# Kernel tuning notes

Measured on AMD Instinct MI355X. Metric: run time of the kernel, lower is better.

The kernel has to match this reference:

```python
import jax, jax.numpy as jnp
import numpy as np

B, T, C, H = 8, 2048, 1024, 64

def setup_inputs() -> dict:
    key = jax.random.key(0)
    kx, kq, kk, kv = jax.random.split(key, 4)
    scale = 1.0 / np.sqrt(C)
    return {
        "x": jax.random.normal(kx, (B, T, C), dtype=jnp.float32),
        "Wq": jax.random.normal(kq, (C, H), dtype=jnp.float32) * scale,
        "Wk": jax.random.normal(kk, (C, H), dtype=jnp.float32) * scale,
        "Wv": jax.random.normal(kv, (C, H), dtype=jnp.float32) * scale,
    }

def reference(x, Wq, Wk, Wv):
    # q,k,v: [B,T,H]
    q = jnp.einsum('btc,ch->bth', x, Wq)
    k = jnp.einsum('btc,ch->bth', x, Wk)
    v = jnp.einsum('btc,ch->bth', x, Wv)
    scale = k.shape[-1] ** -0.5
    wei = jnp.einsum('bth,bsh->bts', q, k) * scale  # [B,T,T]
    causal = jnp.tril(jnp.ones((x.shape[1], x.shape[1]), dtype=bool))
    wei = jnp.where(causal, wei, -jnp.inf)
    wei = jax.nn.softmax(wei, axis=-1)
    out = jnp.einsum('bts,bsh->bth', wei, v)  # [B,T,H]
    return out
```

## Files before the change

kernel.cpp:

```cpp
#include <hip/hip_runtime.h>

#define B_ 8
#define T_ 2048
#define C_ 1024
#define H_ 64

typedef __bf16 bf16x8 __attribute__((ext_vector_type(8)));
typedef float  f32x4  __attribute__((ext_vector_type(4)));
typedef unsigned short u16x8 __attribute__((ext_vector_type(8)));

__device__ __forceinline__ unsigned short f2bf(float f) {
    unsigned u = __builtin_bit_cast(unsigned, f);
    u += 0x8000u;
    return (unsigned short)(u >> 16);
}

__device__ __forceinline__ unsigned pack2(float lo, float hi) {
    unsigned a = __builtin_bit_cast(unsigned, lo) + 0x8000u;
    unsigned b = __builtin_bit_cast(unsigned, hi) + 0x8000u;
    return (a >> 16) | (b & 0xffff0000u);
}

union U8 { unsigned u32[4]; u16x8 v; };

__device__ __forceinline__ u16x8 cvt8(float4 f0, float4 f1) {
    U8 r;
    r.u32[0] = pack2(f0.x, f0.y);
    r.u32[1] = pack2(f0.z, f0.w);
    r.u32[2] = pack2(f1.x, f1.y);
    r.u32[3] = pack2(f1.z, f1.w);
    return r.v;
}

__device__ __forceinline__ bf16x8 load8_bf(const unsigned short* p) {
    return __builtin_bit_cast(bf16x8, *(const u16x8*)p);
}

__global__ void cast_weights(const float* __restrict__ Wq,
                             const float* __restrict__ Wk,
                             const float* __restrict__ Wv,
                             unsigned short* __restrict__ Wt) {
    int idx = blockIdx.x * blockDim.x + threadIdx.x;
    int w   = idx >> 16;
    int rem = idx & 0xffff;
    int c   = rem & (C_ - 1);
    int h   = rem >> 10;
    const float* W = (w == 0) ? Wq : (w == 1) ? Wk : Wv;
    Wt[(size_t)(w * H_ + h) * C_ + c] = f2bf(W[(size_t)c * H_ + h]);
}

#define ABUF (64 * 64)
#define BBUF (192 * 64)

__global__ __launch_bounds__(512) void qkv_proj(
        const float* __restrict__ x,
        const unsigned short* __restrict__ Wt,
        unsigned short* __restrict__ Qb,
        unsigned short* __restrict__ Kb,
        unsigned short* __restrict__ VTb) {
    __shared__ __attribute__((aligned(16))) unsigned short As_[2 * ABUF];
    __shared__ __attribute__((aligned(16))) unsigned short Bs_[2 * BBUF];

    const int tid  = threadIdx.x;
    const int wave = tid >> 6;
    const int lane = tid & 63;
    const int l16  = lane & 15;
    const int quad = lane >> 4;
    const int ms   = wave >> 1;
    const int nh   = wave & 1;
    const size_t r0 = (size_t)blockIdx.x * 64;

    const int sa_m = tid >> 3, sa_g = tid & 7;
    const float* sa_src = x + (r0 + sa_m) * C_ + sa_g * 8;
    const int sa_off = sa_m * 64 + ((sa_g ^ (sa_m & 7)) * 8);

    f32x4 acc[6];
#pragma unroll
    for (int i = 0; i < 6; i++) acc[i] = (f32x4){0.f, 0.f, 0.f, 0.f};

    const int sw = l16 & 7;

    {
        float4 f0 = *(const float4*)(sa_src);
        float4 f1 = *(const float4*)(sa_src + 4);
        *(u16x8*)(&As_[sa_off]) = cvt8(f0, f1);
#pragma unroll
        for (int p = 0; p < 3; p++) {
            u16x8 v = *(const u16x8*)(Wt + (size_t)(p * 64 + sa_m) * C_ + sa_g * 8);
            *(u16x8*)(&Bs_[p * 4096 + sa_off]) = v;
        }
    }
    __syncthreads();

    int cur = 0;
    for (int ks = 0; ks < 16; ks++) {
        const int k1 = (ks + 1) * 64;
        const bool more = (k1 < C_);
        float4 na0, na1;
        u16x8 nb0, nb1, nb2;
        if (more) {
            na0 = *(const float4*)(sa_src + k1);
            na1 = *(const float4*)(sa_src + k1 + 4);
            nb0 = *(const u16x8*)(Wt + (size_t)(0 * 64 + sa_m) * C_ + k1 + sa_g * 8);
            nb1 = *(const u16x8*)(Wt + (size_t)(1 * 64 + sa_m) * C_ + k1 + sa_g * 8);
            nb2 = *(const u16x8*)(Wt + (size_t)(2 * 64 + sa_m) * C_ + k1 + sa_g * 8);
        }
        const unsigned short* Ac = As_ + cur * ABUF;
        const unsigned short* Bc = Bs_ + cur * BBUF;
        const int arow = ms * 16 + l16;
        bf16x8 a0 = load8_bf(&Ac[arow * 64 + ((quad ^ sw) * 8)]);
        bf16x8 a1 = load8_bf(&Ac[arow * 64 + (((quad + 4) ^ sw) * 8)]);
#pragma unroll
        for (int i = 0; i < 6; i++) {
            int brow = (nh * 6 + i) * 16 + l16;
            bf16x8 b0 = load8_bf(&Bc[brow * 64 + ((quad ^ sw) * 8)]);
            bf16x8 b1 = load8_bf(&Bc[brow * 64 + (((quad + 4) ^ sw) * 8)]);
            acc[i] = __builtin_amdgcn_mfma_f32_16x16x32_bf16(a0, b0, acc[i], 0, 0, 0);
            acc[i] = __builtin_amdgcn_mfma_f32_16x16x32_bf16(a1, b1, acc[i], 0, 0, 0);
        }
        if (more) {
            const int nxt = cur ^ 1;
            *(u16x8*)(&As_[nxt * ABUF + sa_off]) = cvt8(na0, na1);
            *(u16x8*)(&Bs_[nxt * BBUF + 0 * 4096 + sa_off]) = nb0;
            *(u16x8*)(&Bs_[nxt * BBUF + 1 * 4096 + sa_off]) = nb1;
            *(u16x8*)(&Bs_[nxt * BBUF + 2 * 4096 + sa_off]) = nb2;
            __syncthreads();
            cur = nxt;
        }
    }

    const int mrow_base = (int)r0 + ms * 16 + quad * 4;
#pragma unroll
    for (int i = 0; i < 6; i++) {
        int nt = nh * 6 + i;
#pragma unroll
        for (int r = 0; r < 4; r++) {
            int row = mrow_base + r;
            unsigned short bv = f2bf(acc[i][r]);
            if (nt < 4) {
                Qb[(size_t)row * H_ + nt * 16 + l16] = bv;
            } else if (nt < 8) {
                Kb[(size_t)row * H_ + (nt - 4) * 16 + l16] = bv;
            } else {
                int h = (nt - 8) * 16 + l16;
                int b = row >> 11;
                int t = row & (T_ - 1);
                VTb[((size_t)b * H_ + h) * T_ + t] = bv;
            }
        }
    }
}

#define PROW 33
#define OMS  65

__global__ __launch_bounds__(512) void attn(
        const unsigned short* __restrict__ Qb,
        const unsigned short* __restrict__ Kb,
        const unsigned short* __restrict__ VTb,
        float* __restrict__ out) {
    __shared__ unsigned int ps_[8 * 16 * PROW];
    __shared__ float Om_[8 * 16 * OMS];
    __shared__ float mred_[8 * 16];
    __shared__ float lred_[8 * 16];

    const int tid  = threadIdx.x;
    const int wave = tid >> 6;
    const int lane = tid & 63;
    const int l16  = lane & 15;
    const int quad = lane >> 4;
    const int b    = blockIdx.x >> 7;
    const int qt   = blockIdx.x & 127;
    const int q0   = qt * 16;
    const int tdiag = qt >> 2;

    const unsigned short* qrow =
        Qb + ((size_t)b * T_ + q0 + l16) * H_ + quad * 8;
    bf16x8 qf0 = load8_bf(qrow);
    bf16x8 qf1 = load8_bf(qrow + 32);

    f32x4 o[4];
#pragma unroll
    for (int i = 0; i < 4; i++) o[i] = (f32x4){0.f, 0.f, 0.f, 0.f};
    float m_run = -1e30f, l_run = 0.f;

    const float scale = 0.125f;
    const unsigned short* Kbase = Kb + (size_t)b * T_ * H_;
    const unsigned short* Vbase = VTb + (size_t)b * H_ * T_;
    unsigned int* Pw = &ps_[wave * 16 * PROW];

    for (int t = wave; t <= tdiag; t += 8) {
        bf16x8 vf[8];
#pragma unroll
        for (int ht = 0; ht < 4; ht++)
#pragma unroll
            for (int ks = 0; ks < 2; ks++)
                vf[ht * 2 + ks] = load8_bf(
                    Vbase + (size_t)(ht * 16 + l16) * T_ + t * 64 + ks * 32 + quad * 8);

        f32x4 s[4];
#pragma unroll
        for (int nt = 0; nt < 4; nt++) {
            const unsigned short* krow =
                Kbase + (size_t)(t * 64 + nt * 16 + l16) * H_ + quad * 8;
            bf16x8 kf0 = load8_bf(krow);
            bf16x8 kf1 = load8_bf(krow + 32);
            f32x4 z = (f32x4){0.f, 0.f, 0.f, 0.f};
            z = __builtin_amdgcn_mfma_f32_16x16x32_bf16(kf0, qf0, z, 0, 0, 0);
            z = __builtin_amdgcn_mfma_f32_16x16x32_bf16(kf1, qf1, z, 0, 0, 0);
            s[nt] = z;
        }

#pragma unroll
        for (int nt = 0; nt < 4; nt++)
#pragma unroll
            for (int r = 0; r < 4; r++) s[nt][r] *= scale;

        if (t == tdiag) {
#pragma unroll
            for (int nt = 0; nt < 4; nt++) {
#pragma unroll
                for (int r = 0; r < 4; r++) {
                    int key = t * 64 + nt * 16 + quad * 4 + r;
                    if (key > q0 + l16) s[nt][r] = -1e30f;
                }
            }
        }

        float mx;
        {
            float m0 = fmaxf(fmaxf(s[0][0], s[0][1]), fmaxf(s[0][2], s[0][3]));
            float m1 = fmaxf(fmaxf(s[1][0], s[1][1]), fmaxf(s[1][2], s[1][3]));
            float m2 = fmaxf(fmaxf(s[2][0], s[2][1]), fmaxf(s[2][2], s[2][3]));
            float m3 = fmaxf(fmaxf(s[3][0], s[3][1]), fmaxf(s[3][2], s[3][3]));
            mx = fmaxf(fmaxf(m0, m1), fmaxf(m2, m3));
        }
        mx = fmaxf(mx, __shfl_xor(mx, 16));
        mx = fmaxf(mx, __shfl_xor(mx, 32));
        const float m_new = fmaxf(m_run, mx);
        const float alpha = __expf(m_run - m_new);
        m_run = m_new;

        float rs = 0.f;
#pragma unroll
        for (int nt = 0; nt < 4; nt++) {
#pragma unroll
            for (int i = 0; i < 2; i++) {
                float p0 = __expf(s[nt][2 * i]     - m_new);
                float p1 = __expf(s[nt][2 * i + 1] - m_new);
                rs += p0 + p1;
                Pw[l16 * PROW + nt * 8 + quad * 2 + i] = pack2(p0, p1);
            }
        }
        rs += __shfl_xor(rs, 16);
        rs += __shfl_xor(rs, 32);
        l_run = l_run * alpha + rs;

#pragma unroll
        for (int ht = 0; ht < 4; ht++)
#pragma unroll
            for (int r = 0; r < 4; r++) o[ht][r] *= alpha;

#pragma unroll
        for (int ks = 0; ks < 2; ks++) {
            bf16x8 pB = __builtin_bit_cast(bf16x8,
                *(const u16x8*)(&Pw[l16 * PROW + ks * 16 + quad * 4]));
#pragma unroll
            for (int ht = 0; ht < 4; ht++)
                o[ht] = __builtin_amdgcn_mfma_f32_16x16x32_bf16(
                    vf[ht * 2 + ks], pB, o[ht], 0, 0, 0);
        }
    }

#pragma unroll
    for (int ht = 0; ht < 4; ht++)
#pragma unroll
        for (int r = 0; r < 4; r++)
            Om_[(wave * 16 + l16) * OMS + ht * 16 + quad * 4 + r] = o[ht][r];
    if (quad == 0) {
        mred_[wave * 16 + l16] = m_run;
        lred_[wave * 16 + l16] = l_run;
    }
    __syncthreads();

    const int hcol = tid & 63;
    const int qrow0 = tid >> 6;
#pragma unroll
    for (int qq = 0; qq < 2; qq++) {
        const int q = qrow0 + qq * 8;
        float M = -1e30f;
#pragma unroll
        for (int w = 0; w < 8; w++) M = fmaxf(M, mred_[w * 16 + q]);
        float lt = 0.f, ov = 0.f;
#pragma unroll
        for (int w = 0; w < 8; w++) {
            float e = __expf(mred_[w * 16 + q] - M);
            lt += e * lred_[w * 16 + q];
            ov += e * Om_[(w * 16 + q) * OMS + hcol];
        }
        out[((size_t)b * T_ + q0 + q) * H_ + hcol] = ov / lt;
    }
}

extern "C" void kernel_launch(void* const* d_in, const int* in_sizes, int n_in,
                              void* d_out, int out_size, void* d_ws, size_t ws_size,
                              hipStream_t stream) {
    const float* x  = (const float*)d_in[0];
    const float* Wq = (const float*)d_in[1];
    const float* Wk = (const float*)d_in[2];
    const float* Wv = (const float*)d_in[3];
    float* out = (float*)d_out;

    unsigned short* Qb  = (unsigned short*)d_ws;
    unsigned short* Kb  = Qb  + (size_t)B_ * T_ * H_;
    unsigned short* VTb = Kb  + (size_t)B_ * T_ * H_;
    unsigned short* Wt  = VTb + (size_t)B_ * T_ * H_;

    cast_weights<<<(3 * C_ * H_) / 256, 256, 0, stream>>>(Wq, Wk, Wv, Wt);
    qkv_proj<<<(B_ * T_) / 64, 512, 0, stream>>>(x, Wt, Qb, Kb, VTb);
    attn<<<B_ * (T_ / 16), 512, 0, stream>>>(Qb, Kb, VTb, out);
}
```

Measured before the change: 163.7 us.

## Store Q/K/V in MFMA fragment-tiled layout and split projection across N halves

The projection kernel now writes Q, K and V directly in a tiled layout that matches the MFMA fragment order, so the attention kernel's loads become contiguous 1KB chunks instead of strided row reads. The projection grid is also restructured to 32-row, 96-column tiles with 256 threads, giving four times as many smaller blocks. Separately, the cross-wave output reduction buffer in shared memory is stored as bf16 instead of fp32 to cut LDS footprint. The trade-offs are the extra bf16 rounding in the final combine and the x rows being read twice by the two N-half blocks.

```diff
diff --git a/kernel.cpp b/kernel.cpp
--- a/kernel.cpp
+++ b/kernel.cpp
@@ -13,6 +13,11 @@
     unsigned u = __builtin_bit_cast(unsigned, f);
     u += 0x8000u;
     return (unsigned short)(u >> 16);
+}
+
+__device__ __forceinline__ float bf2f(unsigned short v) {
+    unsigned u = ((unsigned)v) << 16;
+    return __builtin_bit_cast(float, u);
 }
 
 __device__ __forceinline__ unsigned pack2(float lo, float hi) {
@@ -35,6 +40,7 @@
 __device__ __forceinline__ bf16x8 load8_bf(const unsigned short* p) {
     return __builtin_bit_cast(bf16x8, *(const u16x8*)p);
 }
+
 
 __global__ void cast_weights(const float* __restrict__ Wq,
                              const float* __restrict__ Wk,
@@ -49,15 +55,15 @@
     Wt[(size_t)(w * H_ + h) * C_ + c] = f2bf(W[(size_t)c * H_ + h]);
 }
 
-#define ABUF (64 * 64)
-#define BBUF (192 * 64)
-
-__global__ __launch_bounds__(512) void qkv_proj(
+#define ABUF 2048
+#define BBUF 6144
+
+__global__ __launch_bounds__(256) void qkv_proj(
         const float* __restrict__ x,
         const unsigned short* __restrict__ Wt,
-        unsigned short* __restrict__ Qb,
-        unsigned short* __restrict__ Kb,
-        unsigned short* __restrict__ VTb) {
+        unsigned short* __restrict__ Qf,
+        unsigned short* __restrict__ Kf,
+        unsigned short* __restrict__ Vf) {
     __shared__ __attribute__((aligned(16))) unsigned short As_[2 * ABUF];
     __shared__ __attribute__((aligned(16))) unsigned short Bs_[2 * BBUF];
 
@@ -67,27 +73,30 @@
     const int l16  = lane & 15;
     const int quad = lane >> 4;
     const int ms   = wave >> 1;
-    const int nh   = wave & 1;
-    const size_t r0 = (size_t)blockIdx.x * 64;
-
-    const int sa_m = tid >> 3, sa_g = tid & 7;
-    const float* sa_src = x + (r0 + sa_m) * C_ + sa_g * 8;
-    const int sa_off = sa_m * 64 + ((sa_g ^ (sa_m & 7)) * 8);
-
-    f32x4 acc[6];
-#pragma unroll
-    for (int i = 0; i < 6; i++) acc[i] = (f32x4){0.f, 0.f, 0.f, 0.f};
+    const int nsub = wave & 1;
+    const int mb   = blockIdx.x >> 1;
+    const int nh   = blockIdx.x & 1;
+    const size_t r0 = (size_t)mb * 32;
+
+    const int srow = tid >> 3, sg = tid & 7;
+    const float* sa_src = x + (r0 + srow) * C_ + sg * 8;
+    const unsigned short* wb = Wt + (size_t)(nh * 96) * C_;
+    const int a_off = srow * 64 + ((sg ^ (srow & 7)) * 8);
+
+    f32x4 acc[3];
+#pragma unroll
+    for (int i = 0; i < 3; i++) acc[i] = (f32x4){0.f, 0.f, 0.f, 0.f};
 
     const int sw = l16 & 7;
 
     {
         float4 f0 = *(const float4*)(sa_src);
         float4 f1 = *(const float4*)(sa_src + 4);
-        *(u16x8*)(&As_[sa_off]) = cvt8(f0, f1);
+        *(u16x8*)(&As_[a_off]) = cvt8(f0, f1);
 #pragma unroll
         for (int p = 0; p < 3; p++) {
-            u16x8 v = *(const u16x8*)(Wt + (size_t)(p * 64 + sa_m) * C_ + sa_g * 8);
-            *(u16x8*)(&Bs_[p * 4096 + sa_off]) = v;
+            u16x8 v = *(const u16x8*)(wb + (size_t)(p * 32 + srow) * C_ + sg * 8);
+            *(u16x8*)(&Bs_[p * 2048 + a_off]) = v;
         }
     }
     __syncthreads();
@@ -101,9 +110,9 @@
         if (more) {
             na0 = *(const float4*)(sa_src + k1);
             na1 = *(const float4*)(sa_src + k1 + 4);
-            nb0 = *(const u16x8*)(Wt + (size_t)(0 * 64 + sa_m) * C_ + k1 + sa_g * 8);
-            nb1 = *(const u16x8*)(Wt + (size_t)(1 * 64 + sa_m) * C_ + k1 + sa_g * 8);
-            nb2 = *(const u16x8*)(Wt + (size_t)(2 * 64 + sa_m) * C_ + k1 + sa_g * 8);
+            nb0 = *(const u16x8*)(wb + (size_t)(0 * 32 + srow) * C_ + k1 + sg * 8);
+            nb1 = *(const u16x8*)(wb + (size_t)(1 * 32 + srow) * C_ + k1 + sg * 8);
+            nb2 = *(const u16x8*)(wb + (size_t)(2 * 32 + srow) * C_ + k1 + sg * 8);
         }
         const unsigned short* Ac = As_ + cur * ABUF;
         const unsigned short* Bc = Bs_ + cur * BBUF;
@@ -111,8 +120,8 @@
         bf16x8 a0 = load8_bf(&Ac[arow * 64 + ((quad ^ sw) * 8)]);
         bf16x8 a1 = load8_bf(&Ac[arow * 64 + (((quad + 4) ^ sw) * 8)]);
 #pragma unroll
-        for (int i = 0; i < 6; i++) {
-            int brow = (nh * 6 + i) * 16 + l16;
+        for (int i = 0; i < 3; i++) {
+            int brow = (nsub * 3 + i) * 16 + l16;
             bf16x8 b0 = load8_bf(&Bc[brow * 64 + ((quad ^ sw) * 8)]);
             bf16x8 b1 = load8_bf(&Bc[brow * 64 + (((quad + 4) ^ sw) * 8)]);
             acc[i] = __builtin_amdgcn_mfma_f32_16x16x32_bf16(a0, b0, acc[i], 0, 0, 0);
@@ -120,47 +129,56 @@
         }
         if (more) {
             const int nxt = cur ^ 1;
-            *(u16x8*)(&As_[nxt * ABUF + sa_off]) = cvt8(na0, na1);
-            *(u16x8*)(&Bs_[nxt * BBUF + 0 * 4096 + sa_off]) = nb0;
-            *(u16x8*)(&Bs_[nxt * BBUF + 1 * 4096 + sa_off]) = nb1;
-            *(u16x8*)(&Bs_[nxt * BBUF + 2 * 4096 + sa_off]) = nb2;
+            *(u16x8*)(&As_[nxt * ABUF + a_off]) = cvt8(na0, na1);
+            *(u16x8*)(&Bs_[nxt * BBUF + 0 * 2048 + a_off]) = nb0;
+            *(u16x8*)(&Bs_[nxt * BBUF + 1 * 2048 + a_off]) = nb1;
+            *(u16x8*)(&Bs_[nxt * BBUF + 2 * 2048 + a_off]) = nb2;
             __syncthreads();
             cur = nxt;
         }
     }
 
-    const int mrow_base = (int)r0 + ms * 16 + quad * 4;
-#pragma unroll
-    for (int i = 0; i < 6; i++) {
-        int nt = nh * 6 + i;
+#pragma unroll
+    for (int i = 0; i < 3; i++) {
+        int nt = nh * 6 + nsub * 3 + i;
 #pragma unroll
         for (int r = 0; r < 4; r++) {
-            int row = mrow_base + r;
+            int row  = (int)r0 + ms * 16 + quad * 4 + r;
+            int bb   = row >> 11;
+            int tloc = row & (T_ - 1);
             unsigned short bv = f2bf(acc[i][r]);
             if (nt < 4) {
-                Qb[(size_t)row * H_ + nt * 16 + l16] = bv;
+                int part  = nt >> 1;
+                int quadf = (nt & 1) * 2 + (l16 >> 3);
+                Qf[((size_t)(bb * 128 + (tloc >> 4)) * 2 + part) * 512
+                   + (tloc & 15) * 32 + quadf * 8 + (l16 & 7)] = bv;
             } else if (nt < 8) {
-                Kb[(size_t)row * H_ + (nt - 4) * 16 + l16] = bv;
+                int nk    = nt - 4;
+                int part  = nk >> 1;
+                int quadf = (nk & 1) * 2 + (l16 >> 3);
+                Kf[((size_t)(bb * 128 + (tloc >> 4)) * 2 + part) * 512
+                   + (tloc & 15) * 32 + quadf * 8 + (l16 & 7)] = bv;
             } else {
-                int h = (nt - 8) * 16 + l16;
-                int b = row >> 11;
-                int t = row & (T_ - 1);
-                VTb[((size_t)b * H_ + h) * T_ + t] = bv;
+                int ht  = nt - 8;
+                int s32 = tloc >> 5;
+                int w32 = tloc & 31;
+                Vf[((size_t)(bb * 64 + s32) * 4 + ht) * 512
+                   + l16 * 32 + (w32 >> 3) * 8 + (w32 & 7)] = bv;
             }
         }
     }
 }
 
 #define PROW 33
-#define OMS  65
+#define OMS2 66
 
 __global__ __launch_bounds__(512) void attn(
-        const unsigned short* __restrict__ Qb,
-        const unsigned short* __restrict__ Kb,
-        const unsigned short* __restrict__ VTb,
+        const unsigned short* __restrict__ Qf,
+        const unsigned short* __restrict__ Kf,
+        const unsigned short* __restrict__ Vf,
         float* __restrict__ out) {
     __shared__ unsigned int ps_[8 * 16 * PROW];
-    __shared__ float Om_[8 * 16 * OMS];
+    __shared__ unsigned short Om_[8 * 16 * OMS2];
     __shared__ float mred_[8 * 16];
     __shared__ float lred_[8 * 16];
 
@@ -174,10 +192,11 @@
     const int q0   = qt * 16;
     const int tdiag = qt >> 2;
 
-    const unsigned short* qrow =
-        Qb + ((size_t)b * T_ + q0 + l16) * H_ + quad * 8;
-    bf16x8 qf0 = load8_bf(qrow);
-    bf16x8 qf1 = load8_bf(qrow + 32);
+    const int loff = l16 * 32 + quad * 8;
+
+    const unsigned short* Qfb = Qf + (size_t)(b * 128 + qt) * 1024;
+    bf16x8 qf0 = load8_bf(Qfb + loff);
+    bf16x8 qf1 = load8_bf(Qfb + 512 + loff);
 
     f32x4 o[4];
 #pragma unroll
@@ -185,26 +204,25 @@
     float m_run = -1e30f, l_run = 0.f;
 
     const float scale = 0.125f;
-    const unsigned short* Kbase = Kb + (size_t)b * T_ * H_;
-    const unsigned short* Vbase = VTb + (size_t)b * H_ * T_;
+    const unsigned short* Kfb = Kf + (size_t)b * 128 * 1024;
+    const unsigned short* Vfb = Vf + (size_t)b * 64 * 2048;
     unsigned int* Pw = &ps_[wave * 16 * PROW];
 
     for (int t = wave; t <= tdiag; t += 8) {
         bf16x8 vf[8];
 #pragma unroll
-        for (int ht = 0; ht < 4; ht++)
-#pragma unroll
-            for (int ks = 0; ks < 2; ks++)
+        for (int ks = 0; ks < 2; ks++)
+#pragma unroll
+            for (int ht = 0; ht < 4; ht++)
                 vf[ht * 2 + ks] = load8_bf(
-                    Vbase + (size_t)(ht * 16 + l16) * T_ + t * 64 + ks * 32 + quad * 8);
+                    Vfb + ((size_t)(t * 2 + ks) * 4 + ht) * 512 + loff);
 
         f32x4 s[4];
 #pragma unroll
         for (int nt = 0; nt < 4; nt++) {
-            const unsigned short* krow =
-                Kbase + (size_t)(t * 64 + nt * 16 + l16) * H_ + quad * 8;
-            bf16x8 kf0 = load8_bf(krow);
-            bf16x8 kf1 = load8_bf(krow + 32);
+            const unsigned short* kp = Kfb + (size_t)(t * 4 + nt) * 1024;
+            bf16x8 kf0 = load8_bf(kp + loff);
+            bf16x8 kf1 = load8_bf(kp + 512 + loff);
             f32x4 z = (f32x4){0.f, 0.f, 0.f, 0.f};
             z = __builtin_amdgcn_mfma_f32_16x16x32_bf16(kf0, qf0, z, 0, 0, 0);
             z = __builtin_amdgcn_mfma_f32_16x16x32_bf16(kf1, qf1, z, 0, 0, 0);
@@ -276,7 +294,7 @@
     for (int ht = 0; ht < 4; ht++)
 #pragma unroll
         for (int r = 0; r < 4; r++)
-            Om_[(wave * 16 + l16) * OMS + ht * 16 + quad * 4 + r] = o[ht][r];
+            Om_[(wave * 16 + l16) * OMS2 + ht * 16 + quad * 4 + r] = f2bf(o[ht][r]);
     if (quad == 0) {
         mred_[wave * 16 + l16] = m_run;
         lred_[wave * 16 + l16] = l_run;
@@ -296,7 +314,7 @@
         for (int w = 0; w < 8; w++) {
             float e = __expf(mred_[w * 16 + q] - M);
             lt += e * lred_[w * 16 + q];
-            ov += e * Om_[(w * 16 + q) * OMS + hcol];
+            ov += e * bf2f(Om_[(w * 16 + q) * OMS2 + hcol]);
         }
         out[((size_t)b * T_ + q0 + q) * H_ + hcol] = ov / lt;
     }
@@ -311,12 +329,12 @@
     const float* Wv = (const float*)d_in[3];
     float* out = (float*)d_out;
 
-    unsigned short* Qb  = (unsigned short*)d_ws;
-    unsigned short* Kb  = Qb  + (size_t)B_ * T_ * H_;
-    unsigned short* VTb = Kb  + (size_t)B_ * T_ * H_;
-    unsigned short* Wt  = VTb + (size_t)B_ * T_ * H_;
+    unsigned short* Qf = (unsigned short*)d_ws;
+    unsigned short* Kf = Qf + (size_t)B_ * T_ * H_;
+    unsigned short* Vf = Kf + (size_t)B_ * T_ * H_;
+    unsigned short* Wt = Vf + (size_t)B_ * T_ * H_;
 
     cast_weights<<<(3 * C_ * H_) / 256, 256, 0, stream>>>(Wq, Wk, Wv, Wt);
-    qkv_proj<<<(B_ * T_) / 64, 512, 0, stream>>>(x, Wt, Qb, Kb, VTb);
-    attn<<<B_ * (T_ / 16), 512, 0, stream>>>(Qb, Kb, VTb, out);
-}
+    qkv_proj<<<(B_ * T_ / 32) * 2, 256, 0, stream>>>(x, Wt, Qf, Kf, Vf);
+    attn<<<B_ * (T_ / 16), 512, 0, stream>>>(Qf, Kf, Vf, out);
+}
```

New measurement: 147.9 us. 1.11x faster.
